# Kernel optimization log

Hardware: AMD Instinct MI355X
Metric: run time of the kernel (lower is better)

## Reference

```python
import jax, jax.numpy as jnp
import numpy as np

N = 100000
E = 1600000
IN_C = 128
OUT_C = 64
ALPHA = 0.2  # LeakyReLU negative slope


def _xavier(key, shape, gain=1.414):
    fan_in, fan_out = shape[-2] if len(shape) > 1 else shape[-1], shape[-1]
    bound = gain * np.sqrt(6.0 / (shape[0] * 0 + (shape[-2] if len(shape) > 1 else 1) + shape[-1])) if False else gain * np.sqrt(6.0 / (sum(shape)))
    return jax.random.uniform(key, shape, jnp.float32, -bound, bound)


def setup_inputs() -> dict:
    key = jax.random.key(0)
    k_x, k_s, k_o, k_w, k_a = jax.random.split(key, 5)
    x = jax.random.normal(k_x, (N, IN_C), jnp.float32)
    # edge list with no self-loops (so remove_self_loops is a no-op)
    src = jax.random.randint(k_s, (E,), 0, N)
    off = jax.random.randint(k_o, (E,), 1, N)
    dst = (src + off) % N
    edge_index = jnp.stack([src, dst]).astype(jnp.int64)
    W = _xavier(k_w, (IN_C, OUT_C))
    a = _xavier(k_a, (1, 2 * OUT_C))
    return {"x": x, "W": W, "a": a, "edge_index": edge_index}


def reference(x, W, a, edge_index):
    h = x @ W                               # [N, D]
    n, d = h.shape
    loops = jnp.arange(n, dtype=edge_index.dtype)
    src = jnp.concatenate([edge_index[0], loops])   # add_self_loops
    dst = jnp.concatenate([edge_index[1], loops])
    # (cat(h[src], h[dst]) * a).sum(-1) == h[src]@a1 + h[dst]@a2
    a1, a2 = a[0, :d], a[0, d:]
    s = h @ a1                              # [N]
    t = h @ a2                              # [N]
    edge_e = jnp.exp(jax.nn.leaky_relu(s[src] + t[dst], negative_slope=ALPHA))  # [E+N]
    e_expsum = jax.ops.segment_sum(edge_e, src, num_segments=n)                  # [N]
    h_prime = jax.ops.segment_sum(edge_e[:, None] * h[dst], src, num_segments=n)  # [N, D]
    return h_prime / e_expsum[:, None]
```

## Files before the change

kernel.cpp:

```cpp
#include <hip/hip_runtime.h>
#include <math.h>

#define IN_C 128
#define OUT_C 64
#define ALPHA 0.2f

#define LDK 136

#define BSH 7
#define NPB 128
#define MAXB 1024
#define PA_EPT 4
#define PA_THREADS 1024
#define PA_TILE (PA_THREADS * PA_EPT)
#define CHUNK 4096

typedef __attribute__((ext_vector_type(8))) short short8;
typedef __attribute__((ext_vector_type(4))) float v4f;

__device__ __forceinline__ ushort f2b(float f) {
  unsigned u = __float_as_uint(f);
  u += 0x7fffu + ((u >> 16) & 1u);
  return (ushort)(u >> 16);
}

__global__ __launch_bounds__(256) void gemm_st_kernel(
    const float* __restrict__ x, const float* __restrict__ W,
    const float* __restrict__ a, ushort* __restrict__ hb,
    float* __restrict__ s, float* __restrict__ t, int* __restrict__ gcur,
    int nbuck, int cape, int n_nodes, int n_tiles) {
  __shared__ ushort xs[64 * LDK];
  __shared__ ushort ws[64 * LDK];

  const int tid = threadIdx.x;
  const int wave = tid >> 6;
  const int lane = tid & 63;
  const int li = lane & 15;
  const int quad = lane >> 4;

  if (blockIdx.x == 0) {
    for (int i = tid; i < nbuck; i += 256) gcur[i] = i * cape;
  }

  for (int i = tid; i < IN_C * OUT_C; i += 256) {
    const int k = i >> 6;
    const int n = i & 63;
    ws[n * LDK + k] = f2b(W[i]);
  }
  __syncthreads();

  short8 bfrag[4][4];
#pragma unroll
  for (int ct = 0; ct < 4; ++ct)
#pragma unroll
    for (int kk = 0; kk < 4; ++kk)
      bfrag[ct][kk] =
          *(const short8*)&ws[(ct * 16 + li) * LDK + kk * 32 + quad * 8];

  float a1v[4], a2v[4];
#pragma unroll
  for (int ct = 0; ct < 4; ++ct) {
    a1v[ct] = a[ct * 16 + li];
    a2v[ct] = a[OUT_C + ct * 16 + li];
  }

  for (int tile = blockIdx.x; tile < n_tiles; tile += gridDim.x) {
    const int row0 = tile * 64;

    __syncthreads();
    for (int i = tid; i < 64 * (IN_C / 4); i += 256) {
      const int r = i >> 5;
      const int c4 = i & 31;
      int row = row0 + r;
      row = row < n_nodes ? row : n_nodes - 1;
      const float4 v = *(const float4*)&x[(size_t)row * IN_C + c4 * 4];
      uint2 p;
      p.x = (unsigned)f2b(v.x) | ((unsigned)f2b(v.y) << 16);
      p.y = (unsigned)f2b(v.z) | ((unsigned)f2b(v.w) << 16);
      *(uint2*)&xs[r * LDK + c4 * 4] = p;
    }
    __syncthreads();

    v4f acc[4];
#pragma unroll
    for (int ct = 0; ct < 4; ++ct) acc[ct] = (v4f){0.f, 0.f, 0.f, 0.f};

    const int rbase = wave * 16;
#pragma unroll
    for (int kk = 0; kk < 4; ++kk) {
      const short8 af =
          *(const short8*)&xs[(rbase + li) * LDK + kk * 32 + quad * 8];
#pragma unroll
      for (int ct = 0; ct < 4; ++ct)
        acc[ct] = __builtin_amdgcn_mfma_f32_16x16x32_bf16(af, bfrag[ct][kk],
                                                          acc[ct], 0, 0, 0);
    }

    const int growbase = row0 + rbase + quad * 4;
    float ps[4] = {0.f, 0.f, 0.f, 0.f};
    float pt[4] = {0.f, 0.f, 0.f, 0.f};
#pragma unroll
    for (int ct = 0; ct < 4; ++ct) {
#pragma unroll
      for (int r = 0; r < 4; ++r) {
        const float hv = acc[ct][r];
        ps[r] += hv * a1v[ct];
        pt[r] += hv * a2v[ct];
        const int grow = growbase + r;
        if (grow < n_nodes)
          hb[(size_t)grow * OUT_C + ct * 16 + li] = f2b(hv);
      }
    }
#pragma unroll
    for (int m = 1; m <= 8; m <<= 1) {
#pragma unroll
      for (int r = 0; r < 4; ++r) {
        ps[r] += __shfl_xor(ps[r], m, 64);
        pt[r] += __shfl_xor(pt[r], m, 64);
      }
    }
    if (li < 4) {
      const int grow = growbase + li;
      if (grow < n_nodes) {
        const float sv = li == 0 ? ps[0] : li == 1 ? ps[1] : li == 2 ? ps[2] : ps[3];
        const float tv = li == 0 ? pt[0] : li == 1 ? pt[1] : li == 2 ? pt[2] : pt[3];
        s[grow] = sv;
        t[grow] = tv;
      }
    }
  }
}

__global__ __launch_bounds__(PA_THREADS) void pa_bin(
    const int* __restrict__ src, const int* __restrict__ dst,
    int* __restrict__ gcur, int* __restrict__ pairs, int nbuck, int cape,
    int E) {
  __shared__ int hist[MAXB];
  __shared__ int cur[MAXB];
  const int tid = threadIdx.x;
  for (int i = tid; i < nbuck; i += PA_THREADS) hist[i] = 0;
  __syncthreads();

  const int e0 = blockIdx.x * PA_TILE + tid * PA_EPT;
  if (e0 + PA_EPT <= E) {
    const int4 v = *(const int4*)(src + e0);
    atomicAdd(&hist[v.x >> BSH], 1);
    atomicAdd(&hist[v.y >> BSH], 1);
    atomicAdd(&hist[v.z >> BSH], 1);
    atomicAdd(&hist[v.w >> BSH], 1);
  } else {
    for (int e = e0; e < E; ++e) atomicAdd(&hist[src[e] >> BSH], 1);
  }
  __syncthreads();

  for (int i = tid; i < nbuck; i += PA_THREADS) {
    const int c = hist[i];
    cur[i] = c ? atomicAdd(&gcur[i], c) : 0;
  }
  __syncthreads();

#define EMIT(sv, dv)                                          \
  {                                                           \
    const int bkt = (sv) >> BSH;                              \
    const int pos = atomicAdd(&cur[bkt], 1);                  \
    if (pos < (bkt + 1) * cape)                               \
      pairs[pos] = (((sv) & (NPB - 1)) << 25) | (dv);         \
  }

  if (e0 + PA_EPT <= E) {
    const int4 sv = *(const int4*)(src + e0);
    const int4 dv = *(const int4*)(dst + e0);
    EMIT(sv.x, dv.x);
    EMIT(sv.y, dv.y);
    EMIT(sv.z, dv.z);
    EMIT(sv.w, dv.w);
  } else {
    for (int e = e0; e < E; ++e) {
      const int sv = src[e];
      const int dv = dst[e];
      EMIT(sv, dv);
    }
  }
#undef EMIT
}

#define ACC8(o, p, wgt)                                      \
  acc[(o) + 0] += (wgt)*__uint_as_float((p).x << 16);        \
  acc[(o) + 1] += (wgt)*__uint_as_float((p).x & 0xffff0000u);\
  acc[(o) + 2] += (wgt)*__uint_as_float((p).y << 16);        \
  acc[(o) + 3] += (wgt)*__uint_as_float((p).y & 0xffff0000u);\
  acc[(o) + 4] += (wgt)*__uint_as_float((p).z << 16);        \
  acc[(o) + 5] += (wgt)*__uint_as_float((p).z & 0xffff0000u);\
  acc[(o) + 6] += (wgt)*__uint_as_float((p).w << 16);        \
  acc[(o) + 7] += (wgt)*__uint_as_float((p).w & 0xffff0000u);

__global__ __launch_bounds__(256) void aggregate_sorted(
    const int* __restrict__ pairs, const int* __restrict__ gcur,
    const uint4* __restrict__ hb4, const float* __restrict__ s,
    const float* __restrict__ t, float* __restrict__ out, int n_nodes,
    int cape) {
  __shared__ int sl[CHUNK];
  __shared__ int cnt[NPB];
  __shared__ int loffs[NPB];
  __shared__ int cur[NPB];
  __shared__ int w0tot_sh;

  const int b = blockIdx.x;
  const int tid = threadIdx.x;
  const int base = b * cape;
  int fill = gcur[b] - base;
  fill = fill < cape ? fill : cape;

  const int local = tid >> 1;
  const int half = tid & 1;
  const int u = b * NPB + local;
  const bool valid = u < n_nodes;
  const float su = valid ? s[u] : 0.f;

  float acc[32];
#pragma unroll
  for (int i = 0; i < 32; ++i) acc[i] = 0.f;
  float den = 0.f;

  for (int c0 = 0; c0 < fill; c0 += CHUNK) {
    const int clen = min(CHUNK, fill - c0);
    if (tid < NPB) cnt[tid] = 0;
    __syncthreads();

    int pw[CHUNK / 256];
#pragma unroll
    for (int j = 0; j < CHUNK / 256; ++j) {
      const int k = j * 256 + tid;
      if (k < clen) {
        pw[j] = pairs[base + c0 + k];
        atomicAdd(&cnt[((unsigned)pw[j]) >> 25], 1);
      }
    }
    __syncthreads();

    int c = 0, incl = 0;
    if (tid < NPB) {
      c = cnt[tid];
      incl = c;
#pragma unroll
      for (int off = 1; off < 64; off <<= 1) {
        const int o = __shfl_up(incl, off, 64);
        if ((tid & 63) >= off) incl += o;
      }
      if (tid == 63) w0tot_sh = incl;
    }
    __syncthreads();
    if (tid < NPB) {
      if (tid >= 64) incl += w0tot_sh;
      loffs[tid] = incl - c;
      cur[tid] = incl - c;
    }
    __syncthreads();

#pragma unroll
    for (int j = 0; j < CHUNK / 256; ++j) {
      const int k = j * 256 + tid;
      if (k < clen) {
        const int lo = ((unsigned)pw[j]) >> 25;
        const int pos = atomicAdd(&cur[lo], 1);
        sl[pos] = pw[j] & 0x1ffffff;
      }
    }
    __syncthreads();

    const int s0 = loffs[local];
    const int s1 = s0 + cnt[local];
    int e = s0;
    for (; e + 1 < s1; e += 2) {
      const int va = sl[e];
      const int vb = sl[e + 1];
      const float ta = t[va];
      const float tb = t[vb];
      const uint4* ra = &hb4[(size_t)va * 8 + half * 4];
      const uint4* rb = &hb4[(size_t)vb * 8 + half * 4];
      const uint4 pa0 = ra[0], pa1 = ra[1], pa2 = ra[2], pa3 = ra[3];
      const uint4 pb0 = rb[0], pb1 = rb[1], pb2 = rb[2], pb3 = rb[3];
      float za = su + ta;
      float zb = su + tb;
      za = za > 0.f ? za : ALPHA * za;
      zb = zb > 0.f ? zb : ALPHA * zb;
      const float wa = __expf(za);
      const float wb = __expf(zb);
      ACC8(0, pa0, wa) ACC8(8, pa1, wa) ACC8(16, pa2, wa) ACC8(24, pa3, wa)
      ACC8(0, pb0, wb) ACC8(8, pb1, wb) ACC8(16, pb2, wb) ACC8(24, pb3, wb)
      den += wa + wb;
    }
    if (e < s1) {
      const int va = sl[e];
      const float ta = t[va];
      const uint4* ra = &hb4[(size_t)va * 8 + half * 4];
      const uint4 pa0 = ra[0], pa1 = ra[1], pa2 = ra[2], pa3 = ra[3];
      float za = su + ta;
      za = za > 0.f ? za : ALPHA * za;
      const float wa = __expf(za);
      ACC8(0, pa0, wa) ACC8(8, pa1, wa) ACC8(16, pa2, wa) ACC8(24, pa3, wa)
      den += wa;
    }
    __syncthreads();
  }

  if (valid) {
    float z0 = su + t[u];
    z0 = z0 > 0.f ? z0 : ALPHA * z0;
    const float w0 = __expf(z0);
    const uint4* rs = &hb4[(size_t)u * 8 + half * 4];
    const uint4 q0 = rs[0], q1 = rs[1], q2 = rs[2], q3 = rs[3];
    ACC8(0, q0, w0) ACC8(8, q1, w0) ACC8(16, q2, w0) ACC8(24, q3, w0)
    den += w0;
    const float inv = 1.f / den;
#pragma unroll
    for (int q = 0; q < 8; ++q) {
      float4 o;
      o.x = acc[q * 4 + 0] * inv;
      o.y = acc[q * 4 + 1] * inv;
      o.z = acc[q * 4 + 2] * inv;
      o.w = acc[q * 4 + 3] * inv;
      *(float4*)&out[(size_t)u * OUT_C + half * 32 + q * 4] = o;
    }
  }
}

extern "C" void kernel_launch(void* const* d_in, const int* in_sizes, int n_in,
                              void* d_out, int out_size, void* d_ws,
                              size_t ws_size, hipStream_t stream) {
  const float* x = (const float*)d_in[0];
  const float* W = (const float*)d_in[1];
  const float* a = (const float*)d_in[2];
  const int* edge_index = (const int*)d_in[3];

  const int n_nodes = in_sizes[0] / IN_C;
  const int E = in_sizes[3] / 2;
  const int* src = edge_index;
  const int* dst = edge_index + E;

  float* out = (float*)d_out;

  const int nbuck = (n_nodes + NPB - 1) >> BSH;
  const int cape = (((E + nbuck - 1) / nbuck) + 768 + 15) & ~15;
  const int nblk_bin = (E + PA_TILE - 1) / PA_TILE;

  ushort* hb = (ushort*)d_ws;
  float* s = (float*)(hb + (size_t)n_nodes * OUT_C);
  float* t = s + n_nodes;
  int* gcur = (int*)(t + n_nodes);
  int* pairs = gcur + MAXB;

  {
    const int n_tiles = (n_nodes + 63) / 64;
    const int ngrid = n_tiles < 512 ? n_tiles : 512;
    gemm_st_kernel<<<ngrid, 256, 0, stream>>>(x, W, a, hb, s, t, gcur, nbuck,
                                              cape, n_nodes, n_tiles);
  }

  pa_bin<<<nblk_bin, PA_THREADS, 0, stream>>>(src, dst, gcur, pairs, nbuck,
                                              cape, E);

  aggregate_sorted<<<nbuck, 256, 0, stream>>>(pairs, gcur, (const uint4*)hb, s,
                                              t, out, n_nodes, cape);
}
```

Measured before the change: 188.0 us.

## Coalesce hb stores via LDS staging and locally sort edges before scatter

In the projection kernel, bf16 h values are first written to shared memory and then copied to global memory as full 16-byte row chunks. Before, each lane stored scattered 2-byte values. In the binning kernel, each block now counting-sorts its edge tile by bucket in shared memory using a block-wide prefix scan. It then writes pairs to global memory in bucket order, so consecutive threads write contiguous runs instead of random scattered stores. This costs extra shared memory, more barriers and a scan, and the binning code now assumes nbuck never exceeds the thread count.

```diff
diff --git a/kernel.cpp b/kernel.cpp
--- a/kernel.cpp
+++ b/kernel.cpp
@@ -96,7 +96,6 @@
                                                           acc[ct], 0, 0, 0);
     }
 
-    const int growbase = row0 + rbase + quad * 4;
     float ps[4] = {0.f, 0.f, 0.f, 0.f};
     float pt[4] = {0.f, 0.f, 0.f, 0.f};
 #pragma unroll
@@ -106,9 +105,6 @@
         const float hv = acc[ct][r];
         ps[r] += hv * a1v[ct];
         pt[r] += hv * a2v[ct];
-        const int grow = growbase + r;
-        if (grow < n_nodes)
-          hb[(size_t)grow * OUT_C + ct * 16 + li] = f2b(hv);
       }
     }
 #pragma unroll
@@ -119,6 +115,7 @@
         pt[r] += __shfl_xor(pt[r], m, 64);
       }
     }
+    const int growbase = row0 + rbase + quad * 4;
     if (li < 4) {
       const int grow = growbase + li;
       if (grow < n_nodes) {
@@ -128,6 +125,23 @@
         t[grow] = tv;
       }
     }
+
+    __syncthreads();
+#pragma unroll
+    for (int ct = 0; ct < 4; ++ct)
+#pragma unroll
+      for (int r = 0; r < 4; ++r)
+        xs[(rbase + quad * 4 + r) * LDK + ct * 16 + li] = f2b(acc[ct][r]);
+    __syncthreads();
+    for (int j = tid; j < 64 * 8; j += 256) {
+      const int row = j >> 3;
+      const int u8 = j & 7;
+      const int grow = row0 + row;
+      if (grow < n_nodes) {
+        const uint4 v = *(const uint4*)&xs[row * LDK + u8 * 8];
+        *(uint4*)&hb[(size_t)grow * OUT_C + u8 * 8] = v;
+      }
+    }
   }
 }
 
@@ -136,52 +150,91 @@
     int* __restrict__ gcur, int* __restrict__ pairs, int nbuck, int cape,
     int E) {
   __shared__ int hist[MAXB];
-  __shared__ int cur[MAXB];
+  __shared__ int loffs[MAXB];
+  __shared__ int lcur[MAXB];
+  __shared__ int gbase[MAXB];
+  __shared__ int wsum[16];
+  __shared__ int sl[PA_TILE];
+  __shared__ ushort sbkt[PA_TILE];
+
   const int tid = threadIdx.x;
-  for (int i = tid; i < nbuck; i += PA_THREADS) hist[i] = 0;
-  __syncthreads();
-
-  const int e0 = blockIdx.x * PA_TILE + tid * PA_EPT;
-  if (e0 + PA_EPT <= E) {
-    const int4 v = *(const int4*)(src + e0);
-    atomicAdd(&hist[v.x >> BSH], 1);
-    atomicAdd(&hist[v.y >> BSH], 1);
-    atomicAdd(&hist[v.z >> BSH], 1);
-    atomicAdd(&hist[v.w >> BSH], 1);
+  const int lane = tid & 63;
+  const int wid = tid >> 6;
+  hist[tid] = 0;
+  __syncthreads();
+
+  const int eblk0 = blockIdx.x * PA_TILE;
+  const int nblk_edges = min(PA_TILE, E - eblk0);
+  const int e0 = eblk0 + tid * PA_EPT;
+
+  int4 sv, dv;
+  const bool full = (e0 + PA_EPT <= E);
+  if (full) {
+    sv = *(const int4*)(src + e0);
+    dv = *(const int4*)(dst + e0);
+    atomicAdd(&hist[sv.x >> BSH], 1);
+    atomicAdd(&hist[sv.y >> BSH], 1);
+    atomicAdd(&hist[sv.z >> BSH], 1);
+    atomicAdd(&hist[sv.w >> BSH], 1);
   } else {
     for (int e = e0; e < E; ++e) atomicAdd(&hist[src[e] >> BSH], 1);
   }
   __syncthreads();
 
-  for (int i = tid; i < nbuck; i += PA_THREADS) {
-    const int c = hist[i];
-    cur[i] = c ? atomicAdd(&gcur[i], c) : 0;
-  }
-  __syncthreads();
-
-#define EMIT(sv, dv)                                          \
+  const int c = hist[tid];
+  gbase[tid] = c ? atomicAdd(&gcur[tid], c) : 0;
+
+  int incl = c;
+#pragma unroll
+  for (int off = 1; off < 64; off <<= 1) {
+    const int o = __shfl_up(incl, off, 64);
+    if (lane >= off) incl += o;
+  }
+  if (lane == 63) wsum[wid] = incl;
+  __syncthreads();
+  if (tid < 16) {
+    const int v = wsum[tid];
+    int sc = v;
+#pragma unroll
+    for (int off = 1; off < 16; off <<= 1) {
+      const int o = __shfl_up(sc, off, 64);
+      if (tid >= off) sc += o;
+    }
+    wsum[tid] = sc - v;
+  }
+  __syncthreads();
+  const int excl = incl - c + wsum[wid];
+  loffs[tid] = excl;
+  lcur[tid] = excl;
+  __syncthreads();
+
+#define PUTS(svv, dvv)                                        \
   {                                                           \
-    const int bkt = (sv) >> BSH;                              \
-    const int pos = atomicAdd(&cur[bkt], 1);                  \
-    if (pos < (bkt + 1) * cape)                               \
-      pairs[pos] = (((sv) & (NPB - 1)) << 25) | (dv);         \
-  }
-
-  if (e0 + PA_EPT <= E) {
-    const int4 sv = *(const int4*)(src + e0);
-    const int4 dv = *(const int4*)(dst + e0);
-    EMIT(sv.x, dv.x);
-    EMIT(sv.y, dv.y);
-    EMIT(sv.z, dv.z);
-    EMIT(sv.w, dv.w);
+    const int bkt = (svv) >> BSH;                             \
+    const int pos = atomicAdd(&lcur[bkt], 1);                 \
+    sl[pos] = (((svv) & (NPB - 1)) << 25) | (dvv);            \
+    sbkt[pos] = (ushort)bkt;                                  \
+  }
+  if (full) {
+    PUTS(sv.x, dv.x);
+    PUTS(sv.y, dv.y);
+    PUTS(sv.z, dv.z);
+    PUTS(sv.w, dv.w);
   } else {
     for (int e = e0; e < E; ++e) {
-      const int sv = src[e];
-      const int dv = dst[e];
-      EMIT(sv, dv);
-    }
-  }
-#undef EMIT
+      const int svv = src[e];
+      const int dvv = dst[e];
+      PUTS(svv, dvv);
+    }
+  }
+#undef PUTS
+  __syncthreads();
+
+  for (int k = tid; k < nblk_edges; k += PA_THREADS) {
+    const int bkt = sbkt[k];
+    const int gpos = gbase[bkt] + (k - loffs[bkt]);
+    if (gpos < (bkt + 1) * cape) pairs[gpos] = sl[k];
+  }
 }
 
 #define ACC8(o, p, wgt)                                      \
```

Result: faster. 177.1 us (-5.8%).
